# Kernel optimization log

Hardware: AMD Instinct MI355X
Metric: run time of the kernel (lower is better)

The kernel has to match this reference:

```python
import jax, jax.numpy as jnp
import numpy as np
import math

D_PAIR = 64
N_HEADS = 4
D_HEAD = D_PAIR // N_HEADS


def setup_inputs() -> dict:
    key = jax.random.key(0)
    ks = jax.random.split(key, 9)
    B, L, D = 2, 256, D_PAIR
    s = 1.0 / math.sqrt(D)
    return {
        "z": jax.random.normal(ks[0], (B, L, L, D), dtype=jnp.float32),
        "ln_scale": jnp.ones((D,), jnp.float32),
        "ln_bias": jnp.zeros((D,), jnp.float32),
        "Wq": jax.random.normal(ks[1], (D, D), jnp.float32) * s,
        "Wk": jax.random.normal(ks[2], (D, D), jnp.float32) * s,
        "Wv": jax.random.normal(ks[3], (D, D), jnp.float32) * s,
        "Wg": jax.random.normal(ks[4], (D, D), jnp.float32) * s,
        "bg": jax.random.normal(ks[5], (D,), jnp.float32) * 0.02,
        "Wo": jax.random.normal(ks[6], (D, D), jnp.float32) * s,
        "bo": jax.random.normal(ks[7], (D,), jnp.float32) * 0.02,
    }


def _layernorm(x, scale, bias, eps=1e-5):
    mu = jnp.mean(x, axis=-1, keepdims=True)
    var = jnp.var(x, axis=-1, keepdims=True)
    return (x - mu) * jax.lax.rsqrt(var + eps) * scale + bias


def reference(z, ln_scale, ln_bias, Wq, Wk, Wv, Wg, bg, Wo, bo):
    B, L, _, D = z.shape
    H, Dh = N_HEADS, D_HEAD
    zn = _layernorm(z, ln_scale, ln_bias)
    # torch Linear(no bias): x @ W.T
    Q = (zn @ Wq.T).reshape(B, L, L, H, Dh)
    K = (zn @ Wk.T).reshape(B, L, L, H, Dh)
    V = (zn @ Wv.T).reshape(B, L, L, H, Dh)
    scale = 1.0 / math.sqrt(Dh)
    # row-wise attention: for each row l, attend over column index j
    attn = jnp.einsum("blihd,bljhd->blhij", Q, K) * scale  # [B,L,H,L,L]
    attn = jax.nn.softmax(attn, axis=-1)
    out = jnp.einsum("blhij,bljhd->blihd", attn, V).reshape(B, L, L, D)
    gate = jax.nn.sigmoid(zn @ Wg.T + bg)
    out = gate * out
    return out @ Wo.T + bo
```

## Files before the change

### kernel.cpp

```cpp
#include <hip/hip_runtime.h>
#include <hip/hip_bf16.h>
#include <math.h>


typedef __attribute__((ext_vector_type(4))) float f32x4;
typedef __attribute__((ext_vector_type(8))) short s16x8;

#define MFMA16(a, b, c) __builtin_amdgcn_mfma_f32_16x16x32_bf16((a), (b), (c), 0, 0, 0)

__device__ __forceinline__ unsigned pk2(float a, float b) {
    union { __hip_bfloat162 h; unsigned u; } c;
    float2 t; t.x = a; t.y = b;
    c.h = __float22bfloat162_rn(t);
    return c.u;
}
__device__ __forceinline__ s16x8 cvt8(const float* p) {
    union { unsigned u[4]; s16x8 v; } r;
    r.u[0] = pk2(p[0], p[1]); r.u[1] = pk2(p[2], p[3]);
    r.u[2] = pk2(p[4], p[5]); r.u[3] = pk2(p[6], p[7]);
    return r.v;
}

static constexpr int ZNL = 0;
static constexpr int KSH = 16384;
static constexpr int VT  = 20480;
static constexpr int LDS_EL = 24704;

__global__ __launch_bounds__(256, 3)
void ka_fused(const float* __restrict__ z, const float* __restrict__ ln_s,
              const float* __restrict__ ln_b, const float* __restrict__ Wq,
              const float* __restrict__ Wk, const float* __restrict__ Wv,
              const float* __restrict__ Wg, const float* __restrict__ bg,
              short* __restrict__ ws)
{
    __shared__ __align__(16) short lds[LDS_EL];
    const int tid = threadIdx.x, lane = tid & 63, w = tid >> 6;
    const int n16 = lane & 15, quad = lane >> 4;
    const bool qlo = (quad < 2);
    const int g = blockIdx.x, bl = g >> 2, h = g & 3;
    const size_t rowbase = (size_t)bl * (256 * 64);
    const int wsl = w * 4096;

    {
        float zn[64];
        const float4* zp4 = (const float4*)(z + rowbase + (size_t)tid * 64);
        #pragma unroll
        for (int gq = 0; gq < 16; ++gq) {
            float4 v4 = zp4[gq];
            zn[gq * 4 + 0] = v4.x; zn[gq * 4 + 1] = v4.y;
            zn[gq * 4 + 2] = v4.z; zn[gq * 4 + 3] = v4.w;
        }
        float mu = 0.f;
        #pragma unroll
        for (int k = 0; k < 64; ++k) mu += zn[k];
        mu *= (1.f / 64.f);
        float va = 0.f;
        #pragma unroll
        for (int k = 0; k < 64; ++k) { float d = zn[k] - mu; va += d * d; }
        const float rs = rsqrtf(va * (1.f / 64.f) + 1e-5f);
        #pragma unroll
        for (int k = 0; k < 64; ++k) zn[k] = (zn[k] - mu) * rs * ln_s[k] + ln_b[k];
        const int lr = lane;
        #pragma unroll
        for (int gq = 0; gq < 8; ++gq) {
            union { unsigned u[4]; s16x8 v; } pkv;
            pkv.u[0] = pk2(zn[gq * 8 + 0], zn[gq * 8 + 1]);
            pkv.u[1] = pk2(zn[gq * 8 + 2], zn[gq * 8 + 3]);
            pkv.u[2] = pk2(zn[gq * 8 + 4], zn[gq * 8 + 5]);
            pkv.u[3] = pk2(zn[gq * 8 + 6], zn[gq * 8 + 7]);
            *(s16x8*)&lds[ZNL + wsl + (lr >> 4) * 1024 + (lr & 15) * 64
                          + ((gq ^ (lr & 7)) * 8)] = pkv.v;
        }
    }

    s16x8 bq[2], bk[2], bv[2], bgf[2];
    #pragma unroll
    for (int ks = 0; ks < 2; ++ks) {
        size_t off = (size_t)(h * 16 + n16) * 64 + ks * 32 + quad * 8;
        bq[ks] = cvt8(Wq + off);  bk[ks] = cvt8(Wk + off);
        bv[ks] = cvt8(Wv + off);  bgf[ks] = cvt8(Wg + off);
    }
    const float4 bg4 = *(const float4*)(bg + h * 16 + quad * 4);
    constexpr float QS = 0.25f * 1.44269504088896340736f;

    float g4t[4][4];
    #pragma unroll
    for (int t = 0; t < 4; ++t) {
        s16x8 zn0 = *(const s16x8*)&lds[ZNL + wsl + t * 1024 + n16 * 64
                                        + ((quad ^ (n16 & 7)) * 8)];
        s16x8 zn1 = *(const s16x8*)&lds[ZNL + wsl + t * 1024 + n16 * 64
                                        + (((4 + quad) ^ (n16 & 7)) * 8)];
        f32x4 aq = {}, ak = {}, av = {}, ag = {};
        aq = MFMA16(bq[0], zn0, aq);  aq = MFMA16(bq[1], zn1, aq);
        ak = MFMA16(bk[0], zn0, ak);  ak = MFMA16(bk[1], zn1, ak);
        ag = MFMA16(bgf[0], zn0, ag); ag = MFMA16(bgf[1], zn1, ag);
        av = MFMA16(zn0, bv[0], av);  av = MFMA16(zn1, bv[1], av);
        {
            uint2 p = {pk2(aq[0] * QS, aq[1] * QS), pk2(aq[2] * QS, aq[3] * QS)};
            *(uint2*)&lds[ZNL + wsl + t * 1024 + n16 * 16 + quad * 4] = p;
        }
        {
            uint2 p = {pk2(ak[0], ak[1]), pk2(ak[2], ak[3])};
            *(uint2*)&lds[KSH + (w * 64 + t * 16 + n16) * 16 + quad * 4] = p;
        }
        {
            uint2 p = {pk2(av[0], av[1]), pk2(av[2], av[3])};
            *(uint2*)&lds[VT + n16 * 264 + (w * 64 + t * 16 + quad * 4)] = p;
        }
        #pragma unroll
        for (int r = 0; r < 4; ++r)
            g4t[t][r] = 1.f / (1.f + __expf(-(ag[r] + bg4[r])));
    }

    s16x8 qa[4];
    #pragma unroll
    for (int qt = 0; qt < 4; ++qt) {
        s16x8 q = {};
        if (qlo) q = *(const s16x8*)&lds[ZNL + wsl + qt * 1024 + n16 * 16 + quad * 8];
        qa[qt] = q;
    }
    __syncthreads();

    float lrow[4][4];
    f32x4 o4[4];
    #pragma unroll
    for (int qt = 0; qt < 4; ++qt) {
        o4[qt] = {};
        #pragma unroll
        for (int r = 0; r < 4; ++r) lrow[qt][r] = 0.f;
    }
    const int sw = (n16 ^ (n16 >> 2)) & 3;
    for (int ch = 0; ch < 8; ++ch) {
        #pragma unroll
        for (int jtl = 0; jtl < 2; ++jtl) {
            int jt = ch * 2 + jtl;
            s16x8 kf = {};
            if (qlo) kf = *(const s16x8*)&lds[KSH + (jt * 16 + n16) * 16 + quad * 8];
            const int po = (((jtl * 2 + (quad >> 1)) ^ sw) * 8) + (quad & 1) * 4;
            #pragma unroll
            for (int qt = 0; qt < 4; ++qt) {
                f32x4 zc = {};
                f32x4 s = MFMA16(kf, qa[qt], zc);
                float e0 = exp2f(s[0]), e1 = exp2f(s[1]);
                float e2 = exp2f(s[2]), e3 = exp2f(s[3]);
                lrow[qt][0] += e0; lrow[qt][1] += e1;
                lrow[qt][2] += e2; lrow[qt][3] += e3;
                uint2 p = {pk2(e0, e1), pk2(e2, e3)};
                *(uint2*)&lds[ZNL + wsl + qt * 1024 + 256 + n16 * 40 + po] = p;
            }
        }
        s16x8 vf = *(const s16x8*)&lds[VT + n16 * 264 + ch * 32 + quad * 8];
        #pragma unroll
        for (int qt = 0; qt < 4; ++qt) {
            s16x8 pf = *(const s16x8*)&lds[ZNL + wsl + qt * 1024 + 256 + n16 * 40
                                           + ((quad ^ sw) * 8)];
            o4[qt] = MFMA16(vf, pf, o4[qt]);
        }
    }

    #pragma unroll
    for (int qt = 0; qt < 4; ++qt) {
        float l = lrow[qt][0] + lrow[qt][1] + lrow[qt][2] + lrow[qt][3];
        l += __shfl_xor(l, 16);
        l += __shfl_xor(l, 32);
        const float inv = 1.f / l;
        float g0 = g4t[qt][0] * o4[qt][0] * inv;
        float g1 = g4t[qt][1] * o4[qt][1] * inv;
        float g2 = g4t[qt][2] * o4[qt][2] * inv;
        float g3 = g4t[qt][3] * o4[qt][3] * inv;
        uint2 p = {pk2(g0, g1), pk2(g2, g3)};
        short* dst = ws + (((size_t)h * 512 + bl) * 256 + w * 64 + qt * 16 + n16) * 16
                     + quad * 4;
        *(uint2*)dst = p;
    }
}

__global__ __launch_bounds__(256, 4)
void k3_out(const short* __restrict__ ws, const float* __restrict__ Wo,
            const float* __restrict__ bo, float* __restrict__ out)
{
    const int tid = threadIdx.x, lane = tid & 63, w = tid >> 6;
    const int n16 = lane & 15, quad = lane >> 4;
    const short* GO = ws;
    const int bl = blockIdx.x >> 1, half = blockIdx.x & 1;
    const int rowloc = half * 128 + w * 32;

    s16x8 bfr[4][2];
    #pragma unroll
    for (int nt = 0; nt < 4; ++nt)
        #pragma unroll
        for (int ks = 0; ks < 2; ++ks)
            bfr[nt][ks] = cvt8(Wo + (size_t)(nt * 16 + n16) * 64 + ks * 32 + quad * 8);

    f32x4 acc[2][4] = {};
    #pragma unroll
    for (int mt = 0; mt < 2; ++mt) {
        #pragma unroll
        for (int c = 0; c < 2; ++c) {
            int hp = c * 2 + (quad >> 1);
            const short* ap = &GO[(((size_t)hp * 512 + bl) * 256 + rowloc + mt * 16 + n16) * 16
                                  + (quad & 1) * 8];
            s16x8 a = *(const s16x8*)ap;
            #pragma unroll
            for (int nt = 0; nt < 4; ++nt)
                acc[mt][nt] = MFMA16(a, bfr[nt][c], acc[mt][nt]);
        }
    }
    #pragma unroll
    for (int nt = 0; nt < 4; ++nt) {
        float bov = bo[nt * 16 + n16];
        #pragma unroll
        for (int mt = 0; mt < 2; ++mt)
            #pragma unroll
            for (int r = 0; r < 4; ++r)
                out[((size_t)bl * 256 + rowloc + mt * 16 + quad * 4 + r) * 64 + nt * 16 + n16] =
                    acc[mt][nt][r] + bov;
    }
}

extern "C" void kernel_launch(void* const* d_in, const int* in_sizes, int n_in,
                              void* d_out, int out_size, void* d_ws, size_t ws_size,
                              hipStream_t stream) {
    const float* z  = (const float*)d_in[0];
    const float* ls = (const float*)d_in[1];
    const float* lb = (const float*)d_in[2];
    const float* Wq = (const float*)d_in[3];
    const float* Wk = (const float*)d_in[4];
    const float* Wv = (const float*)d_in[5];
    const float* Wg = (const float*)d_in[6];
    const float* bg = (const float*)d_in[7];
    const float* Wo = (const float*)d_in[8];
    const float* bo = (const float*)d_in[9];
    float* out = (float*)d_out;
    short* wsp = (short*)d_ws;

    hipLaunchKernelGGL(ka_fused, dim3(2048), dim3(256), 0, stream,
                       z, ls, lb, Wq, Wk, Wv, Wg, bg, wsp);
    hipLaunchKernelGGL(k3_out, dim3(1024), dim3(256), 0, stream, wsp, Wo, bo, out);
}
```

Baseline: 172.9 us.

## Shrink per-wave LDS slice with staged row stores to fit four blocks per CU

```diff
diff --git a/kernel.cpp b/kernel.cpp
--- a/kernel.cpp
+++ b/kernel.cpp
@@ -7,6 +7,8 @@
 typedef __attribute__((ext_vector_type(8))) short s16x8;
 
 #define MFMA16(a, b, c) __builtin_amdgcn_mfma_f32_16x16x32_bf16((a), (b), (c), 0, 0, 0)
+#define EXP2R(x) __builtin_amdgcn_exp2f(x)
+#define RCPR(x)  __builtin_amdgcn_rcpf(x)
 
 __device__ __forceinline__ unsigned pk2(float a, float b) {
     union { __hip_bfloat162 h; unsigned u; } c;
@@ -21,12 +23,13 @@
     return r.v;
 }
 
+static constexpr int WSLICE = 2560;
 static constexpr int ZNL = 0;
-static constexpr int KSH = 16384;
-static constexpr int VT  = 20480;
-static constexpr int LDS_EL = 24704;
-
-__global__ __launch_bounds__(256, 3)
+static constexpr int KSH = 10240;
+static constexpr int VT  = 14336;
+static constexpr int LDS_EL = 18560;
+
+__global__ __launch_bounds__(256, 4)
 void ka_fused(const float* __restrict__ z, const float* __restrict__ ln_s,
               const float* __restrict__ ln_b, const float* __restrict__ Wq,
               const float* __restrict__ Wk, const float* __restrict__ Wv,
@@ -39,8 +42,9 @@
     const bool qlo = (quad < 2);
     const int g = blockIdx.x, bl = g >> 2, h = g & 3;
     const size_t rowbase = (size_t)bl * (256 * 64);
-    const int wsl = w * 4096;
-
+    const int wsl = w * WSLICE;
+
+    union { unsigned u[32]; s16x8 v8[8]; } row;
     {
         float zn[64];
         const float4* zp4 = (const float4*)(z + rowbase + (size_t)tid * 64);
@@ -60,18 +64,16 @@
         const float rs = rsqrtf(va * (1.f / 64.f) + 1e-5f);
         #pragma unroll
         for (int k = 0; k < 64; ++k) zn[k] = (zn[k] - mu) * rs * ln_s[k] + ln_b[k];
-        const int lr = lane;
-        #pragma unroll
-        for (int gq = 0; gq < 8; ++gq) {
-            union { unsigned u[4]; s16x8 v; } pkv;
-            pkv.u[0] = pk2(zn[gq * 8 + 0], zn[gq * 8 + 1]);
-            pkv.u[1] = pk2(zn[gq * 8 + 2], zn[gq * 8 + 3]);
-            pkv.u[2] = pk2(zn[gq * 8 + 4], zn[gq * 8 + 5]);
-            pkv.u[3] = pk2(zn[gq * 8 + 6], zn[gq * 8 + 7]);
-            *(s16x8*)&lds[ZNL + wsl + (lr >> 4) * 1024 + (lr & 15) * 64
-                          + ((gq ^ (lr & 7)) * 8)] = pkv.v;
-        }
-    }
+        #pragma unroll
+        for (int k = 0; k < 32; ++k) row.u[k] = pk2(zn[2 * k], zn[2 * k + 1]);
+    }
+
+    auto store_row = [&](int slot) {
+        #pragma unroll
+        for (int gq = 0; gq < 8; ++gq)
+            *(s16x8*)&lds[ZNL + wsl + slot * 1024 + (lane & 15) * 64
+                          + ((gq ^ (lane & 7)) * 8)] = row.v8[gq];
+    };
 
     s16x8 bq[2], bk[2], bv[2], bgf[2];
     #pragma unroll
@@ -82,13 +84,14 @@
     }
     const float4 bg4 = *(const float4*)(bg + h * 16 + quad * 4);
     constexpr float QS = 0.25f * 1.44269504088896340736f;
+    constexpr float L2E = 1.44269504088896340736f;
 
     float g4t[4][4];
-    #pragma unroll
-    for (int t = 0; t < 4; ++t) {
-        s16x8 zn0 = *(const s16x8*)&lds[ZNL + wsl + t * 1024 + n16 * 64
+    s16x8 qa[4];
+    auto proj_tile = [&](int t, int s) {
+        s16x8 zn0 = *(const s16x8*)&lds[ZNL + wsl + s * 1024 + n16 * 64
                                         + ((quad ^ (n16 & 7)) * 8)];
-        s16x8 zn1 = *(const s16x8*)&lds[ZNL + wsl + t * 1024 + n16 * 64
+        s16x8 zn1 = *(const s16x8*)&lds[ZNL + wsl + s * 1024 + n16 * 64
                                         + (((4 + quad) ^ (n16 & 7)) * 8)];
         f32x4 aq = {}, ak = {}, av = {}, ag = {};
         aq = MFMA16(bq[0], zn0, aq);  aq = MFMA16(bq[1], zn1, aq);
@@ -97,7 +100,7 @@
         av = MFMA16(zn0, bv[0], av);  av = MFMA16(zn1, bv[1], av);
         {
             uint2 p = {pk2(aq[0] * QS, aq[1] * QS), pk2(aq[2] * QS, aq[3] * QS)};
-            *(uint2*)&lds[ZNL + wsl + t * 1024 + n16 * 16 + quad * 4] = p;
+            *(uint2*)&lds[ZNL + wsl + 2048 + n16 * 16 + quad * 4] = p;
         }
         {
             uint2 p = {pk2(ak[0], ak[1]), pk2(ak[2], ak[3])};
@@ -109,16 +112,19 @@
         }
         #pragma unroll
         for (int r = 0; r < 4; ++r)
-            g4t[t][r] = 1.f / (1.f + __expf(-(ag[r] + bg4[r])));
-    }
-
-    s16x8 qa[4];
-    #pragma unroll
-    for (int qt = 0; qt < 4; ++qt) {
+            g4t[t][r] = RCPR(1.f + EXP2R(-(ag[r] + bg4[r]) * L2E));
         s16x8 q = {};
-        if (qlo) q = *(const s16x8*)&lds[ZNL + wsl + qt * 1024 + n16 * 16 + quad * 8];
-        qa[qt] = q;
-    }
+        if (qlo) q = *(const s16x8*)&lds[ZNL + wsl + 2048 + n16 * 16 + quad * 8];
+        qa[t] = q;
+    };
+
+    if (lane < 32) store_row(lane >> 4);
+    proj_tile(0, 0);
+    if (lane >= 32 && lane < 48) store_row(0);
+    proj_tile(1, 1);
+    if (lane >= 48) store_row(1);
+    proj_tile(2, 0);
+    proj_tile(3, 1);
     __syncthreads();
 
     float lrow[4][4];
@@ -141,18 +147,18 @@
             for (int qt = 0; qt < 4; ++qt) {
                 f32x4 zc = {};
                 f32x4 s = MFMA16(kf, qa[qt], zc);
-                float e0 = exp2f(s[0]), e1 = exp2f(s[1]);
-                float e2 = exp2f(s[2]), e3 = exp2f(s[3]);
+                float e0 = EXP2R(s[0]), e1 = EXP2R(s[1]);
+                float e2 = EXP2R(s[2]), e3 = EXP2R(s[3]);
                 lrow[qt][0] += e0; lrow[qt][1] += e1;
                 lrow[qt][2] += e2; lrow[qt][3] += e3;
                 uint2 p = {pk2(e0, e1), pk2(e2, e3)};
-                *(uint2*)&lds[ZNL + wsl + qt * 1024 + 256 + n16 * 40 + po] = p;
+                *(uint2*)&lds[ZNL + wsl + qt * 640 + n16 * 40 + po] = p;
             }
         }
         s16x8 vf = *(const s16x8*)&lds[VT + n16 * 264 + ch * 32 + quad * 8];
         #pragma unroll
         for (int qt = 0; qt < 4; ++qt) {
-            s16x8 pf = *(const s16x8*)&lds[ZNL + wsl + qt * 1024 + 256 + n16 * 40
+            s16x8 pf = *(const s16x8*)&lds[ZNL + wsl + qt * 640 + n16 * 40
                                            + ((quad ^ sw) * 8)];
             o4[qt] = MFMA16(vf, pf, o4[qt]);
         }
@@ -163,7 +169,7 @@
         float l = lrow[qt][0] + lrow[qt][1] + lrow[qt][2] + lrow[qt][3];
         l += __shfl_xor(l, 16);
         l += __shfl_xor(l, 32);
-        const float inv = 1.f / l;
+        const float inv = RCPR(l);
         float g0 = g4t[qt][0] * o4[qt][0] * inv;
         float g1 = g4t[qt][1] * o4[qt][1] * inv;
         float g2 = g4t[qt][2] * o4[qt][2] * inv;
```

Result: slower. 312.9 us (+81.0%).
